# Performance work log

Hardware: AMD Instinct MI355X
Metric: run time of the kernel (lower is better)

The kernel has to match this reference:

```python
import jax, jax.numpy as jnp
import numpy as np
import math

DIM = 1024
B, S = 4, 2048

def setup_inputs() -> dict:
    key = jax.random.key(0)
    ks = jax.random.split(key, 4)
    scale = 1.0 / math.sqrt(DIM)
    X = jax.random.normal(ks[0], (B, S, DIM), dtype=jnp.float32)
    W_in = jax.random.normal(ks[1], (3 * DIM, DIM), dtype=jnp.float32) * scale
    b_in = jnp.zeros((3 * DIM,), dtype=jnp.float32)
    W_out = jax.random.normal(ks[2], (DIM, DIM), dtype=jnp.float32) * scale
    b_out = jnp.zeros((DIM,), dtype=jnp.float32)
    attention_mask = jnp.ones((B, 1, S), dtype=jnp.int32)
    return {"X": X, "attention_mask": attention_mask, "W_in": W_in,
            "b_in": b_in, "W_out": W_out, "b_out": b_out}

def reference(X, attention_mask, W_in, b_in, W_out, b_out):
    # in_proj: [B,S,3*DIM]
    qkv = jnp.einsum('bsd,ed->bse', X, W_in) + b_in
    Q, K, V = jnp.split(qkv, 3, axis=-1)
    # scores: [B,S,S]
    scores = jnp.einsum('bqd,bkd->bqk', Q, K)
    # masked_fill happens BEFORE the /sqrt(dim) scaling in the original
    scores = jnp.where(attention_mask == 0, jnp.float32(-1e20), scores)
    attn = jax.nn.softmax(scores / jnp.float32(math.sqrt(DIM)), axis=-1)
    # Dropout(0.1) treated as identity (eval-mode reference)
    out = jnp.einsum('bqk,bkd->bqd', attn, V)
    return jnp.einsum('bsd,od->bso', out, W_out) + b_out
```

## Files before the change

kernel.cpp:

```cpp
#include <hip/hip_runtime.h>
#include <stdint.h>

#define AS1 __attribute__((address_space(1)))
#define AS3 __attribute__((address_space(3)))

typedef __bf16 bf16x8 __attribute__((ext_vector_type(8)));
typedef float f32x16 __attribute__((ext_vector_type(16)));

__device__ __forceinline__ unsigned short f2bf(float f) {
  unsigned u = __float_as_uint(f);
  u += 0x7FFF + ((u >> 16) & 1);
  return (unsigned short)(u >> 16);
}

__global__ __launch_bounds__(256) void cast_all_kernel(const float* __restrict__ X,
                                                       const float* __restrict__ Wi,
                                                       const float* __restrict__ Wo,
                                                       unsigned short* __restrict__ out) {
  const int c1 = 2097152;
  const int c2 = 786432;
  const int c3 = 262144;
  const int total = c1 + c2 + c3;
  for (int i = blockIdx.x * 256 + threadIdx.x; i < total; i += 2048 * 256) {
    const float* src;
    int j = i;
    if (i < c1) src = X;
    else if (i < c1 + c2) { src = Wi; j = i - c1; }
    else { src = Wo; j = i - c1 - c2; }
    float4 v = reinterpret_cast<const float4*>(src)[j];
    ushort4 o;
    o.x = f2bf(v.x); o.y = f2bf(v.y); o.z = f2bf(v.z); o.w = f2bf(v.w);
    reinterpret_cast<ushort4*>(out)[i] = o;
  }
}

template<int MODE>
__global__ __launch_bounds__(256, 2) void gemm_bt128(
    const unsigned short* __restrict__ A, long lda, long strideA,
    const unsigned short* __restrict__ B, long ldb, long strideB,
    void* __restrict__ Cv, long ldc, long strideC,
    const float* __restrict__ bias, const int* __restrict__ mask,
    float* __restrict__ sums, unsigned short* __restrict__ vt, int K) {
  __shared__ unsigned short sA[128 * 64];
  __shared__ unsigned short sB[128 * 64];
  const int t = threadIdx.x;
  const int lane = t & 63;
  const int wave = t >> 6;

  const unsigned short* Ab = A + (size_t)blockIdx.z * strideA + (size_t)blockIdx.y * 128 * lda;
  const unsigned short* Bb = B + (size_t)blockIdx.z * strideB + (size_t)blockIdx.x * 128 * ldb;

  const int srow = t >> 3;
  const int schunk = (t & 7) ^ ((srow >> 1) & 7);
  const unsigned short* aptr = Ab + (size_t)srow * lda + schunk * 8;
  const unsigned short* bptr = Bb + (size_t)srow * ldb + schunk * 8;
  char* ldsA0 = (char*)&sA[0] + wave * 1024;
  char* ldsB0 = (char*)&sB[0] + wave * 1024;

  f32x16 acc[2][2];
#pragma unroll
  for (int i = 0; i < 2; i++)
#pragma unroll
    for (int j = 0; j < 2; j++)
#pragma unroll
      for (int r = 0; r < 16; r++) acc[i][j][r] = 0.f;

  const int wm = (wave >> 1) * 64;
  const int wn = (wave & 1) * 64;
  const int r31 = lane & 31;
  const int half = lane >> 5;
  const int swz = (r31 >> 1) & 7;

  int offA[2][4], offB[2][4];
#pragma unroll
  for (int i = 0; i < 2; i++)
#pragma unroll
    for (int s = 0; s < 4; s++) {
      offA[i][s] = (wm + i * 32 + r31) * 128 + (((2 * s + half) ^ swz) * 16);
      offB[i][s] = (wn + i * 32 + r31) * 128 + (((2 * s + half) ^ swz) * 16);
    }

  for (int k0 = 0; k0 < K; k0 += 64) {
    __syncthreads();
#pragma unroll
    for (int o = 0; o < 4; o++) {
      __builtin_amdgcn_global_load_lds((AS1 void*)(aptr + (size_t)o * 32 * lda + k0),
                                       (AS3 void*)(ldsA0 + o * 4096), 16, 0, 0);
      __builtin_amdgcn_global_load_lds((AS1 void*)(bptr + (size_t)o * 32 * ldb + k0),
                                       (AS3 void*)(ldsB0 + o * 4096), 16, 0, 0);
    }
    __syncthreads();
#pragma unroll
    for (int s = 0; s < 4; s++) {
      bf16x8 af[2], bfv[2];
#pragma unroll
      for (int i = 0; i < 2; i++) {
        af[i]  = *reinterpret_cast<const bf16x8*>((const char*)sA + offA[i][s]);
        bfv[i] = *reinterpret_cast<const bf16x8*>((const char*)sB + offB[i][s]);
      }
#pragma unroll
      for (int i = 0; i < 2; i++)
#pragma unroll
        for (int j = 0; j < 2; j++)
          acc[i][j] = __builtin_amdgcn_mfma_f32_32x32x16_bf16(af[i], bfv[j], acc[i][j], 0, 0, 0);
    }
  }

  const int* mrow = (MODE == 2) ? (mask + (size_t)blockIdx.z * 2048) : nullptr;
  const bool vblock = (MODE == 1) && (blockIdx.x >= 16);
  float rs[2][16];

#pragma unroll
  for (int i = 0; i < 2; i++) {
    int gmb = blockIdx.y * 128 + wm + i * 32;
    float inv_r[16];
    if (MODE == 3) {
#pragma unroll
      for (int r = 0; r < 16; r++) {
        int row = (r & 3) + 8 * (r >> 2) + 4 * half;
        inv_r[r] = 1.0f / sums[(size_t)blockIdx.z * 2048 + gmb + row];
      }
    }
    if (MODE == 2) {
#pragma unroll
      for (int r = 0; r < 16; r++) rs[i][r] = 0.f;
    }
#pragma unroll
    for (int j = 0; j < 2; j++) {
      int gn = blockIdx.x * 128 + wn + j * 32 + r31;
      float bv = (MODE == 0 || MODE == 1) ? bias[gn] : 0.0f;
      if (MODE == 1 && vblock) {
        int b = gmb >> 11;
        int sbase = gmb & 2047;
        int d = gn - 2048;
        unsigned short* vp = vt + (size_t)b * 1024 * 2048 + (size_t)d * 2048 + sbase + 4 * half;
#pragma unroll
        for (int qd = 0; qd < 4; qd++) {
          ushort4 o;
          o.x = f2bf(acc[i][j][4 * qd + 0] + bv);
          o.y = f2bf(acc[i][j][4 * qd + 1] + bv);
          o.z = f2bf(acc[i][j][4 * qd + 2] + bv);
          o.w = f2bf(acc[i][j][4 * qd + 3] + bv);
          *reinterpret_cast<ushort4*>(vp + 8 * qd) = o;
        }
      } else {
        bool msk = (MODE == 2) ? (mrow[gn] == 0) : false;
#pragma unroll
        for (int r = 0; r < 16; r++) {
          int row = (r & 3) + 8 * (r >> 2) + 4 * half;
          float val = acc[i][j][r] + bv;
          size_t off = (size_t)blockIdx.z * strideC + (size_t)(gmb + row) * ldc + gn;
          if (MODE == 2) {
            if (msk) val = -1e20f;
            val = __expf(val * 0.03125f);
            rs[i][r] += val;
            ((unsigned short*)Cv)[off] = f2bf(val);
          } else if (MODE == 3) {
            ((unsigned short*)Cv)[off] = f2bf(val * inv_r[r]);
          } else if (MODE == 1) {
            ((unsigned short*)Cv)[off] = f2bf(val);
          } else {
            ((float*)Cv)[off] = val;
          }
        }
      }
    }
  }

  if (MODE == 2) {
    float* srow2 = sums + (size_t)blockIdx.z * 2048;
#pragma unroll
    for (int i = 0; i < 2; i++) {
      int gmb = blockIdx.y * 128 + wm + i * 32;
#pragma unroll
      for (int r = 0; r < 16; r++) {
        float v = rs[i][r];
#pragma unroll
        for (int o = 16; o >= 1; o >>= 1) v += __shfl_xor(v, o, 64);
        if (r31 == 0) {
          int row = (r & 3) + 8 * (r >> 2) + 4 * half;
          atomicAdd(&srow2[gmb + row], v);
        }
      }
    }
  }
}

extern "C" void kernel_launch(void* const* d_in, const int* in_sizes, int n_in,
                              void* d_out, int out_size, void* d_ws, size_t ws_size,
                              hipStream_t stream) {
  const float* X = (const float*)d_in[0];
  const int* mask = (const int*)d_in[1];
  const float* W_in = (const float*)d_in[2];
  const float* b_in = (const float*)d_in[3];
  const float* W_out = (const float*)d_in[4];
  const float* b_out = (const float*)d_in[5];
  float* out = (float*)d_out;

  const int S = 2048, D = 1024;
  char* w = (char*)d_ws;
  unsigned short* Xb  = (unsigned short*)w;
  unsigned short* Wib = (unsigned short*)(w + 16777216);
  unsigned short* Wob = (unsigned short*)(w + 16777216 + 6291456);
  unsigned short* QK  = (unsigned short*)(w + 25165824);
  unsigned short* P   = (unsigned short*)(w + 58720256);
  unsigned short* Vt  = (unsigned short*)(w + 92274688);
  float*          sums = (float*)(w + 109051904);
  unsigned short* Ob  = Xb;

  hipMemsetAsync(sums, 0, 8192 * sizeof(float), stream);

  cast_all_kernel<<<2048, 256, 0, stream>>>(X, W_in, W_out, Xb);

  gemm_bt128<1><<<dim3(24, 64, 1), 256, 0, stream>>>(
      Xb, D, 0, Wib, D, 0, QK, 2048, 0, b_in, nullptr, nullptr, Vt, D);
  gemm_bt128<2><<<dim3(16, 16, 4), 256, 0, stream>>>(
      QK, 2048, (long)S * 2048, QK + 1024, 2048, (long)S * 2048,
      P, S, (long)S * S, nullptr, mask, sums, nullptr, D);
  gemm_bt128<3><<<dim3(8, 16, 4), 256, 0, stream>>>(
      P, S, (long)S * S, Vt, S, (long)D * S,
      Ob, D, (long)S * D, nullptr, nullptr, sums, nullptr, S);
  gemm_bt128<0><<<dim3(8, 64, 1), 256, 0, stream>>>(
      Ob, D, 0, Wob, D, 0, out, D, 0, b_out, nullptr, nullptr, nullptr, D);
}
```

Before: 291.5 us.

## Double K-tile depth to 128 and remap workgroups across XCDs

The GEMM K-step grows from 64 to 128, so each tile gets half as many barrier pairs and global-to-LDS load phases. LDS per block doubles to 64 KB, which may limit two blocks per CU. Workgroup IDs are also remapped so consecutive tiles land on the same XCD (orig&7 chunking), aiming to improve L2 reuse of shared A/B panels. The remap assumes the tile count is divisible by 8, which holds for all launched grids.

```diff
diff --git a/kernel.cpp b/kernel.cpp
--- a/kernel.cpp
+++ b/kernel.cpp
@@ -41,17 +41,24 @@
     void* __restrict__ Cv, long ldc, long strideC,
     const float* __restrict__ bias, const int* __restrict__ mask,
     float* __restrict__ sums, unsigned short* __restrict__ vt, int K) {
-  __shared__ unsigned short sA[128 * 64];
-  __shared__ unsigned short sB[128 * 64];
+  __shared__ unsigned short sA[128 * 128];
+  __shared__ unsigned short sB[128 * 128];
   const int t = threadIdx.x;
   const int lane = t & 63;
   const int wave = t >> 6;
 
-  const unsigned short* Ab = A + (size_t)blockIdx.z * strideA + (size_t)blockIdx.y * 128 * lda;
-  const unsigned short* Bb = B + (size_t)blockIdx.z * strideB + (size_t)blockIdx.x * 128 * ldb;
-
-  const int srow = t >> 3;
-  const int schunk = (t & 7) ^ ((srow >> 1) & 7);
+  const int nx = gridDim.x;
+  const int nwg = nx * gridDim.y;
+  const int orig = blockIdx.y * nx + blockIdx.x;
+  const int qc = nwg >> 3;
+  const int wg = (orig & 7) * qc + (orig >> 3);
+  const int bx = wg % nx, by = wg / nx, bz = blockIdx.z;
+
+  const unsigned short* Ab = A + (size_t)bz * strideA + (size_t)by * 128 * lda;
+  const unsigned short* Bb = B + (size_t)bz * strideB + (size_t)bx * 128 * ldb;
+
+  const int srow = t >> 4;
+  const int schunk = (t & 15) ^ ((srow >> 1) & 7);
   const unsigned short* aptr = Ab + (size_t)srow * lda + schunk * 8;
   const unsigned short* bptr = Bb + (size_t)srow * ldb + schunk * 8;
   char* ldsA0 = (char*)&sA[0] + wave * 1024;
@@ -71,32 +78,33 @@
   const int half = lane >> 5;
   const int swz = (r31 >> 1) & 7;
 
-  int offA[2][4], offB[2][4];
-#pragma unroll
-  for (int i = 0; i < 2; i++)
-#pragma unroll
-    for (int s = 0; s < 4; s++) {
-      offA[i][s] = (wm + i * 32 + r31) * 128 + (((2 * s + half) ^ swz) * 16);
-      offB[i][s] = (wn + i * 32 + r31) * 128 + (((2 * s + half) ^ swz) * 16);
-    }
-
-  for (int k0 = 0; k0 < K; k0 += 64) {
+  int chunkOff[8];
+#pragma unroll
+  for (int s = 0; s < 8; s++) chunkOff[s] = (((2 * s + half) ^ swz) << 4);
+  int rowA[2], rowB[2];
+#pragma unroll
+  for (int i = 0; i < 2; i++) {
+    rowA[i] = (wm + i * 32 + r31) << 8;
+    rowB[i] = (wn + i * 32 + r31) << 8;
+  }
+
+  for (int k0 = 0; k0 < K; k0 += 128) {
     __syncthreads();
 #pragma unroll
-    for (int o = 0; o < 4; o++) {
-      __builtin_amdgcn_global_load_lds((AS1 void*)(aptr + (size_t)o * 32 * lda + k0),
+    for (int o = 0; o < 8; o++) {
+      __builtin_amdgcn_global_load_lds((AS1 void*)(aptr + (size_t)o * 16 * lda + k0),
                                        (AS3 void*)(ldsA0 + o * 4096), 16, 0, 0);
-      __builtin_amdgcn_global_load_lds((AS1 void*)(bptr + (size_t)o * 32 * ldb + k0),
+      __builtin_amdgcn_global_load_lds((AS1 void*)(bptr + (size_t)o * 16 * ldb + k0),
                                        (AS3 void*)(ldsB0 + o * 4096), 16, 0, 0);
     }
     __syncthreads();
 #pragma unroll
-    for (int s = 0; s < 4; s++) {
+    for (int s = 0; s < 8; s++) {
       bf16x8 af[2], bfv[2];
 #pragma unroll
       for (int i = 0; i < 2; i++) {
-        af[i]  = *reinterpret_cast<const bf16x8*>((const char*)sA + offA[i][s]);
-        bfv[i] = *reinterpret_cast<const bf16x8*>((const char*)sB + offB[i][s]);
+        af[i]  = *reinterpret_cast<const bf16x8*>((const char*)sA + rowA[i] + chunkOff[s]);
+        bfv[i] = *reinterpret_cast<const bf16x8*>((const char*)sB + rowB[i] + chunkOff[s]);
       }
 #pragma unroll
       for (int i = 0; i < 2; i++)
@@ -106,19 +114,19 @@
     }
   }
 
-  const int* mrow = (MODE == 2) ? (mask + (size_t)blockIdx.z * 2048) : nullptr;
-  const bool vblock = (MODE == 1) && (blockIdx.x >= 16);
+  const int* mrow = (MODE == 2) ? (mask + (size_t)bz * 2048) : nullptr;
+  const bool vblock = (MODE == 1) && (bx >= 16);
   float rs[2][16];
 
 #pragma unroll
   for (int i = 0; i < 2; i++) {
-    int gmb = blockIdx.y * 128 + wm + i * 32;
+    int gmb = by * 128 + wm + i * 32;
     float inv_r[16];
     if (MODE == 3) {
 #pragma unroll
       for (int r = 0; r < 16; r++) {
         int row = (r & 3) + 8 * (r >> 2) + 4 * half;
-        inv_r[r] = 1.0f / sums[(size_t)blockIdx.z * 2048 + gmb + row];
+        inv_r[r] = 1.0f / sums[(size_t)bz * 2048 + gmb + row];
       }
     }
     if (MODE == 2) {
@@ -127,7 +135,7 @@
     }
 #pragma unroll
     for (int j = 0; j < 2; j++) {
-      int gn = blockIdx.x * 128 + wn + j * 32 + r31;
+      int gn = bx * 128 + wn + j * 32 + r31;
       float bv = (MODE == 0 || MODE == 1) ? bias[gn] : 0.0f;
       if (MODE == 1 && vblock) {
         int b = gmb >> 11;
@@ -149,7 +157,7 @@
         for (int r = 0; r < 16; r++) {
           int row = (r & 3) + 8 * (r >> 2) + 4 * half;
           float val = acc[i][j][r] + bv;
-          size_t off = (size_t)blockIdx.z * strideC + (size_t)(gmb + row) * ldc + gn;
+          size_t off = (size_t)bz * strideC + (size_t)(gmb + row) * ldc + gn;
           if (MODE == 2) {
             if (msk) val = -1e20f;
             val = __expf(val * 0.03125f);
@@ -168,10 +176,10 @@
   }
 
   if (MODE == 2) {
-    float* srow2 = sums + (size_t)blockIdx.z * 2048;
+    float* srow2 = sums + (size_t)bz * 2048;
 #pragma unroll
     for (int i = 0; i < 2; i++) {
-      int gmb = blockIdx.y * 128 + wm + i * 32;
+      int gmb = by * 128 + wm + i * 32;
 #pragma unroll
       for (int r = 0; r < 16; r++) {
         float v = rs[i][r];
```

Measured after the change: 296.7 us. Within noise of the previous version (+1.8%).

## Double-buffer LDS tiles to overlap global loads with MFMA compute

Applied to the files above, without the earlier changes.

The GEMM kernel now has two LDS buffers for the A and B tiles. It issues the global-to-LDS load for the next K slice before running the MFMAs on the current slice, so there is one barrier per iteration instead of two. The aim is to hide global memory latency behind matrix compute in all four GEMM stages. The cost is double the LDS per block (64 KB), which could reduce occupancy if fewer blocks fit per CU.

```diff
diff --git a/kernel.cpp b/kernel.cpp
--- a/kernel.cpp
+++ b/kernel.cpp
@@ -35,14 +35,14 @@
 }
 
 template<int MODE>
-__global__ __launch_bounds__(256, 2) void gemm_bt128(
+__global__ __launch_bounds__(256, 2) void gemm_db(
     const unsigned short* __restrict__ A, long lda, long strideA,
     const unsigned short* __restrict__ B, long ldb, long strideB,
     void* __restrict__ Cv, long ldc, long strideC,
     const float* __restrict__ bias, const int* __restrict__ mask,
     float* __restrict__ sums, unsigned short* __restrict__ vt, int K) {
-  __shared__ unsigned short sA[128 * 64];
-  __shared__ unsigned short sB[128 * 64];
+  __shared__ unsigned short sA[2 * 128 * 64];
+  __shared__ unsigned short sB[2 * 128 * 64];
   const int t = threadIdx.x;
   const int lane = t & 63;
   const int wave = t >> 6;
@@ -54,8 +54,18 @@
   const int schunk = (t & 7) ^ ((srow >> 1) & 7);
   const unsigned short* aptr = Ab + (size_t)srow * lda + schunk * 8;
   const unsigned short* bptr = Bb + (size_t)srow * ldb + schunk * 8;
-  char* ldsA0 = (char*)&sA[0] + wave * 1024;
-  char* ldsB0 = (char*)&sB[0] + wave * 1024;
+
+  auto stage = [&](int k0, int s) {
+    char* dA = (char*)&sA[0] + s * 16384 + wave * 1024;
+    char* dB = (char*)&sB[0] + s * 16384 + wave * 1024;
+#pragma unroll
+    for (int o = 0; o < 4; o++) {
+      __builtin_amdgcn_global_load_lds((AS1 void*)(aptr + (size_t)o * 32 * lda + k0),
+                                       (AS3 void*)(dA + o * 4096), 16, 0, 0);
+      __builtin_amdgcn_global_load_lds((AS1 void*)(bptr + (size_t)o * 32 * ldb + k0),
+                                       (AS3 void*)(dB + o * 4096), 16, 0, 0);
+    }
+  };
 
   f32x16 acc[2][2];
 #pragma unroll
@@ -80,23 +90,21 @@
       offB[i][s] = (wn + i * 32 + r31) * 128 + (((2 * s + half) ^ swz) * 16);
     }
 
+  stage(0, 0);
+  __syncthreads();
+
+  int cur = 0;
   for (int k0 = 0; k0 < K; k0 += 64) {
-    __syncthreads();
-#pragma unroll
-    for (int o = 0; o < 4; o++) {
-      __builtin_amdgcn_global_load_lds((AS1 void*)(aptr + (size_t)o * 32 * lda + k0),
-                                       (AS3 void*)(ldsA0 + o * 4096), 16, 0, 0);
-      __builtin_amdgcn_global_load_lds((AS1 void*)(bptr + (size_t)o * 32 * ldb + k0),
-                                       (AS3 void*)(ldsB0 + o * 4096), 16, 0, 0);
-    }
-    __syncthreads();
+    if (k0 + 64 < K) stage(k0 + 64, cur ^ 1);
+    const char* bufA = (const char*)&sA[0] + cur * 16384;
+    const char* bufB = (const char*)&sB[0] + cur * 16384;
 #pragma unroll
     for (int s = 0; s < 4; s++) {
       bf16x8 af[2], bfv[2];
 #pragma unroll
       for (int i = 0; i < 2; i++) {
-        af[i]  = *reinterpret_cast<const bf16x8*>((const char*)sA + offA[i][s]);
-        bfv[i] = *reinterpret_cast<const bf16x8*>((const char*)sB + offB[i][s]);
+        af[i]  = *reinterpret_cast<const bf16x8*>(bufA + offA[i][s]);
+        bfv[i] = *reinterpret_cast<const bf16x8*>(bufB + offB[i][s]);
       }
 #pragma unroll
       for (int i = 0; i < 2; i++)
@@ -104,6 +112,8 @@
         for (int j = 0; j < 2; j++)
           acc[i][j] = __builtin_amdgcn_mfma_f32_32x32x16_bf16(af[i], bfv[j], acc[i][j], 0, 0, 0);
     }
+    __syncthreads();
+    cur ^= 1;
   }
 
   const int* mrow = (MODE == 2) ? (mask + (size_t)blockIdx.z * 2048) : nullptr;
@@ -212,14 +222,14 @@
 
   cast_all_kernel<<<2048, 256, 0, stream>>>(X, W_in, W_out, Xb);
 
-  gemm_bt128<1><<<dim3(24, 64, 1), 256, 0, stream>>>(
+  gemm_db<1><<<dim3(24, 64, 1), 256, 0, stream>>>(
       Xb, D, 0, Wib, D, 0, QK, 2048, 0, b_in, nullptr, nullptr, Vt, D);
-  gemm_bt128<2><<<dim3(16, 16, 4), 256, 0, stream>>>(
+  gemm_db<2><<<dim3(16, 16, 4), 256, 0, stream>>>(
       QK, 2048, (long)S * 2048, QK + 1024, 2048, (long)S * 2048,
       P, S, (long)S * S, nullptr, mask, sums, nullptr, D);
-  gemm_bt128<3><<<dim3(8, 16, 4), 256, 0, stream>>>(
+  gemm_db<3><<<dim3(8, 16, 4), 256, 0, stream>>>(
       P, S, (long)S * S, Vt, S, (long)D * S,
       Ob, D, (long)S * D, nullptr, nullptr, sums, nullptr, S);
-  gemm_bt128<0><<<dim3(8, 64, 1), 256, 0, stream>>>(
+  gemm_db<0><<<dim3(8, 64, 1), 256, 0, stream>>>(
       Ob, D, 0, Wob, D, 0, out, D, 0, b_out, nullptr, nullptr, nullptr, D);
 }
```

New measurement: 301.4 us. 1.03x slower.
